# Performance work log

Hardware: AMD Instinct MI355X
Metric: run time of the kernel (lower is better)

## Reference

```python
import jax, jax.numpy as jnp
import numpy as np
import math

B, S, HID, H = 4, 2048, 1024, 16
D = HID // H


def setup_inputs() -> dict:
    key = jax.random.key(0)
    ks = jax.random.split(key, 13)
    xavier = lambda k: jax.random.normal(k, (HID, HID), jnp.float32) * math.sqrt(2.0 / (HID + HID))
    return {
        "q": jax.random.normal(ks[0], (B, S, HID), jnp.float32),
        "k": jax.random.normal(ks[1], (B, S, HID), jnp.float32),
        "v": jax.random.normal(ks[2], (B, S, HID), jnp.float32),
        "padding_mask": jax.random.randint(ks[3], (B, S), 0, 2, jnp.int32),
        "Wq": xavier(ks[4]), "bq": jnp.zeros((HID,), jnp.float32),
        "Wk": xavier(ks[5]), "bk": jnp.zeros((HID,), jnp.float32),
        "Wv": xavier(ks[6]), "bv": jnp.zeros((HID,), jnp.float32),
        "Wo": xavier(ks[7]), "bo": jnp.zeros((HID,), jnp.float32),
        "is_causal": 1,
    }


def reference(q, k, v, padding_mask, Wq, bq, Wk, bk, Wv, bv, Wo, bo, is_causal):
    b, s, _ = q.shape
    # torch Linear: y = x @ W.T + b; reshape to [B, H, S, D]
    proj = lambda x, W, bias: (x @ W.T + bias).reshape(b, s, H, D).transpose(0, 2, 1, 3)
    qh, kh, vh = proj(q, Wq, bq), proj(k, Wk, bk), proj(v, Wv, bv)
    corr = jnp.einsum("bhqd,bhkd->bhqk", qh, kh) / math.sqrt(D)  # [B,H,S,S]
    # padding_mask.view(B,1,S,1): masks QUERY rows where mask == 0 (faithful to source)
    corr = jnp.where(padding_mask[:, None, :, None] == 0, jnp.float32(-1e9), corr)
    if is_causal:
        # triu -inf above diagonal; where(...) equals corr + (-inf) at masked slots
        tri = jnp.triu(jnp.ones((s, s), bool), k=1)
        corr = jnp.where(tri[None, None], -jnp.inf, corr)
    prob = jax.nn.softmax(corr, axis=-1)  # dropout p=0 (eval)
    hidden = jnp.einsum("bhqk,bhkd->bhqd", prob, vh)  # [B,H,S,D]
    hidden = hidden.transpose(0, 2, 1, 3).reshape(b, s, H * D)
    return hidden @ Wo.T + bo
```

## Files before the change

### kernel.cpp

```cpp
#include <hip/hip_runtime.h>
#include <hip/hip_bf16.h>
#include <stdint.h>

typedef __attribute__((ext_vector_type(8))) short bf16x8;
typedef __attribute__((ext_vector_type(4))) float f32x4;
typedef __attribute__((ext_vector_type(16))) float f32x16;
typedef __attribute__((ext_vector_type(8))) unsigned short ushort8;
typedef __attribute__((ext_vector_type(4))) unsigned short ushort4v;
typedef __attribute__((ext_vector_type(4))) unsigned int u32x4;
typedef __attribute__((ext_vector_type(2))) unsigned int u32x2;

#define DEVINL __device__ __forceinline__

static constexpr int BB  = 4;
static constexpr int SS  = 2048;
static constexpr int HID = 1024;
static constexpr int NH  = 16;
static constexpr int DH  = 64;

DEVINL unsigned short f2bf(float f) {
  unsigned u = __builtin_bit_cast(unsigned, f);
  u += 0x7fffu + ((u >> 16) & 1u);
  return (unsigned short)(u >> 16);
}

DEVINL unsigned cvt_pk_bf16(float lo, float hi) {
  unsigned r;
  asm("v_cvt_pk_bf16_f32 %0, %1, %2" : "=v"(r) : "v"(lo), "v"(hi));
  return r;
}

DEVINL void gload_lds16(const void* g, void* lds) {
  __builtin_amdgcn_global_load_lds(
      (__attribute__((address_space(1))) unsigned int*)(g),
      (__attribute__((address_space(3))) unsigned int*)(lds), 16, 0, 0);
}

__global__ void cvt4_weights(const float* __restrict__ a,
                             const float* __restrict__ b,
                             const float* __restrict__ c,
                             const float* __restrict__ d,
                             unsigned short* __restrict__ dst) {
  int which = blockIdx.x >> 10;
  const float* src = which == 0 ? a : which == 1 ? b : which == 2 ? c : d;
  int i = ((blockIdx.x & 1023) * 256 + threadIdx.x) * 4;
  float4 v = *(const float4*)(src + i);
  ushort4v h;
  h.x = f2bf(v.x); h.y = f2bf(v.y); h.z = f2bf(v.z); h.w = f2bf(v.w);
  *(ushort4v*)(dst + which * 1048576 + i) = h;
}

template <int A_F32, int OUT_F32>
__launch_bounds__(256)
__global__ void gemm_bt(const void* __restrict__ Ap,
                        const unsigned short* __restrict__ Bw,
                        const float* __restrict__ bias,
                        void* __restrict__ Cp, int M, int N, int K,
                        float oscale) {
  __shared__ __align__(16) unsigned char As[16384];
  __shared__ __align__(16) unsigned char Bs[16384];
  const int cpx = gridDim.x >> 3;
  const int bid = (blockIdx.x & 7) * cpx + (blockIdx.x >> 3);
  const int nb = N >> 7;
  const int bm = bid / nb, bn = bid % nb;
  const int m0 = bm << 7, n0 = bn << 7;
  const int t = threadIdx.x, lane = t & 63, wv = t >> 6;
  const int wr = wv >> 1, wc = wv & 1;
  const int l15 = lane & 15, l4 = lane >> 4;

  f32x4 acc[4][4] = {};

  for (int k0 = 0; k0 < K; k0 += 64) {
#pragma unroll
    for (int j = 0; j < 4; ++j) {
      int p = (wv * 4 + j) * 1024 + lane * 16;
      int row = p >> 7;
      int cb = (p & 127) ^ ((row & 7) << 4);
      gload_lds16(Bw + (size_t)(n0 + row) * K + k0 + (cb >> 1),
                  Bs + (wv * 4 + j) * 1024);
    }
    if (A_F32) {
      const float* Af = (const float*)Ap;
#pragma unroll
      for (int j = 0; j < 8; ++j) {
        int qid = t + j * 256;
        int row = qid >> 4;
        int q16 = qid & 15;
        float4 v = *(const float4*)(Af + (size_t)(m0 + row) * K + k0 + q16 * 4);
        u32x2 w;
        w.x = cvt_pk_bf16(v.x, v.y);
        w.y = cvt_pk_bf16(v.z, v.w);
        int byte = (row * 128 + q16 * 8) ^ ((row & 7) << 4);
        *(u32x2*)(As + byte) = w;
      }
    } else {
      const unsigned short* Ab = (const unsigned short*)Ap;
#pragma unroll
      for (int j = 0; j < 4; ++j) {
        int p = (wv * 4 + j) * 1024 + lane * 16;
        int row = p >> 7;
        int cb = (p & 127) ^ ((row & 7) << 4);
        gload_lds16(Ab + (size_t)(m0 + row) * K + k0 + (cb >> 1),
                    As + (wv * 4 + j) * 1024);
      }
    }
    asm volatile("s_waitcnt vmcnt(0)" ::: "memory");
    __syncthreads();

    bf16x8 af[2][4], bfr[2][4];
#pragma unroll
    for (int kh = 0; kh < 2; ++kh) {
#pragma unroll
      for (int m = 0; m < 4; ++m) {
        int r = wr * 64 + m * 16 + l15;
        int byte = (r * 128 + kh * 64 + l4 * 16) ^ ((r & 7) << 4);
        af[kh][m] = *(const bf16x8*)(As + byte);
      }
#pragma unroll
      for (int n = 0; n < 4; ++n) {
        int r = wc * 64 + n * 16 + l15;
        int byte = (r * 128 + kh * 64 + l4 * 16) ^ ((r & 7) << 4);
        bfr[kh][n] = *(const bf16x8*)(Bs + byte);
      }
    }
#pragma unroll
    for (int kh = 0; kh < 2; ++kh)
#pragma unroll
      for (int m = 0; m < 4; ++m)
#pragma unroll
        for (int n = 0; n < 4; ++n)
          acc[m][n] = __builtin_amdgcn_mfma_f32_16x16x32_bf16(
              af[kh][m], bfr[kh][n], acc[m][n], 0, 0, 0);
    __syncthreads();
  }

#pragma unroll
  for (int n = 0; n < 4; ++n) {
    int col = n0 + wc * 64 + n * 16 + l15;
    float bc = bias[col];
#pragma unroll
    for (int m = 0; m < 4; ++m) {
      int rowb = m0 + wr * 64 + m * 16 + l4 * 4;
#pragma unroll
      for (int r = 0; r < 4; ++r) {
        float val = (acc[m][n][r] + bc) * oscale;
        if (OUT_F32)
          ((float*)Cp)[(size_t)(rowb + r) * N + col] = val;
        else
          ((unsigned short*)Cp)[(size_t)(rowb + r) * N + col] = f2bf(val);
      }
    }
  }
}

__launch_bounds__(256)
__global__ void transpose_v(const unsigned short* __restrict__ Vh,
                            unsigned short* __restrict__ Vt) {
  __shared__ unsigned short Ts[64][65];
  const int bid = blockIdx.x;
  const int st = bid & 31, h = (bid >> 5) & 15, b = bid >> 9;
  const int s0 = st << 6;
  const int t = threadIdx.x;
  {
    int si = t >> 2, jq = (t & 3) * 16;
    const unsigned short* src =
        Vh + ((size_t)(b * SS + s0 + si)) * HID + h * DH + jq;
    ushort8 v0 = *(const ushort8*)src;
    ushort8 v1 = *(const ushort8*)(src + 8);
#pragma unroll
    for (int e = 0; e < 8; ++e) {
      Ts[si][jq + e] = v0[e];
      Ts[si][jq + 8 + e] = v1[e];
    }
  }
  __syncthreads();
  {
    int d = t >> 2, sq = (t & 3) * 16;
    ushort8 o0, o1;
#pragma unroll
    for (int e = 0; e < 8; ++e) {
      o0[e] = Ts[sq + e][d];
      o1[e] = Ts[sq + 8 + e][d];
    }
    unsigned short* dst =
        Vt + ((size_t)((b * NH + h) * DH + d)) * SS + s0 + sq;
    *(ushort8*)dst = o0;
    *(ushort8*)(dst + 8) = o1;
  }
}

__launch_bounds__(256)
__global__ void attn_kernel(const unsigned short* __restrict__ Qh,
                            const unsigned short* __restrict__ Kh,
                            const unsigned short* __restrict__ Vt,
                            const int* __restrict__ pad,
                            const int* __restrict__ pcausal,
                            unsigned short* __restrict__ Out) {
  __shared__ __align__(16) unsigned char Ks[2][8192];
  __shared__ __align__(16) unsigned char Vs[2][8192];
  const int bid = (blockIdx.x & 7) * 64 + (blockIdx.x >> 3);
  const int pr = bid & 7, h = (bid >> 3) & 15, b = bid >> 7;
  const int t = threadIdx.x, lane = t & 63, wv = t >> 6;
  const int l31 = lane & 31, hi = lane >> 5;
  const int causal = *pcausal;
  const int sw = (l31 & 7) << 4;

  for (int half = 0; half < 2; ++half) {
    const int qt = half ? (15 - pr) : pr;
    const int q0 = qt << 7;
    const int qrow = q0 + wv * 32 + l31;
    const bool padded = (pad[b * SS + qrow] == 0);

    const unsigned short* Qb = Qh + ((size_t)(b * SS) + qrow) * HID + h * DH;
    bf16x8 qf[4];
#pragma unroll
    for (int dd = 0; dd < 4; ++dd) {
      qf[dd] = *(const bf16x8*)(Qb + dd * 16 + hi * 8);
      if (padded) qf[dd] = (bf16x8)0;
    }

    f32x16 oacc[2] = {};
    float m = -__builtin_inff(), l = 0.f;
    const int nkt = causal ? (2 * qt + 2) : (SS >> 6);

    auto STAGE = [&](int kt, int s) {
#pragma unroll
      for (int j = 0; j < 2; ++j) {
        int pb = (wv * 2 + j) * 1024 + lane * 16;
        int r_ = pb >> 7;
        int cb = (pb & 127) ^ ((r_ & 7) << 4);
        gload_lds16(Kh + ((size_t)(b * SS) + (kt << 6) + r_) * HID + h * DH +
                        (cb >> 1),
                    Ks[s] + (wv * 2 + j) * 1024);
        gload_lds16(Vt + ((size_t)((b * NH + h) * DH + r_)) * SS + (kt << 6) +
                        (cb >> 1),
                    Vs[s] + (wv * 2 + j) * 1024);
      }
    };

    if (half) __syncthreads();
    STAGE(0, 0);
    for (int kt = 0; kt < nkt; ++kt) {
      asm volatile("s_waitcnt vmcnt(0)" ::: "memory");
      __syncthreads();
      if (kt + 1 < nkt) STAGE(kt + 1, (kt + 1) & 1);
      const unsigned char* Kb = Ks[kt & 1];
      const unsigned char* Vb = Vs[kt & 1];
      const int k0 = kt << 6;

      const bool active = (!causal) || (k0 <= q0 + wv * 32 + 31);
      if (active) {
        f32x16 sacc[2] = {};
#pragma unroll
        for (int kb = 0; kb < 2; ++kb) {
#pragma unroll
          for (int dd = 0; dd < 4; ++dd) {
            int krow = kb * 32 + l31;
            int byte = (krow * 128 + dd * 32 + hi * 16) ^ sw;
            bf16x8 kf = *(const bf16x8*)(Kb + byte);
            sacc[kb] = __builtin_amdgcn_mfma_f32_32x32x16_bf16(kf, qf[dd],
                                                               sacc[kb], 0, 0, 0);
          }
        }
        if (causal && (k0 + 63 > q0 + wv * 32)) {
#pragma unroll
          for (int kb = 0; kb < 2; ++kb)
#pragma unroll
            for (int r = 0; r < 16; ++r) {
              int kidx = k0 + kb * 32 + (r & 3) + 8 * (r >> 2) + 4 * hi;
              if (kidx > qrow) sacc[kb][r] = -__builtin_inff();
            }
        }
        float ta = fmaxf(sacc[0][0], sacc[0][1]);
        float tb = fmaxf(sacc[0][2], sacc[0][3]);
#pragma unroll
        for (int r = 4; r < 16; r += 4) {
          ta = fmaxf(ta, fmaxf(sacc[0][r], sacc[0][r + 1]));
          tb = fmaxf(tb, fmaxf(sacc[0][r + 2], sacc[0][r + 3]));
        }
#pragma unroll
        for (int r = 0; r < 16; r += 4) {
          ta = fmaxf(ta, fmaxf(sacc[1][r], sacc[1][r + 1]));
          tb = fmaxf(tb, fmaxf(sacc[1][r + 2], sacc[1][r + 3]));
        }
        float tmax = fmaxf(ta, tb);
        tmax = fmaxf(tmax, __shfl_xor(tmax, 32));
        if (__any(tmax > m + 8.0f)) {
          float mnew = fmaxf(m, tmax);
          float corr = __builtin_amdgcn_exp2f(m - mnew);
          m = mnew;
          l *= corr;
#pragma unroll
          for (int db = 0; db < 2; ++db)
#pragma unroll
            for (int r = 0; r < 16; ++r) oacc[db][r] *= corr;
        }
        float ls = 0.f;
#pragma unroll
        for (int kb = 0; kb < 2; ++kb)
#pragma unroll
          for (int r = 0; r < 16; ++r) {
            float p = __builtin_amdgcn_exp2f(sacc[kb][r] - m);
            sacc[kb][r] = p;
            ls += p;
          }
        l += ls;

        bf16x8 pf[4];
#pragma unroll
        for (int kb = 0; kb < 2; ++kb) {
          unsigned w0 = cvt_pk_bf16(sacc[kb][0], sacc[kb][1]);
          unsigned w1 = cvt_pk_bf16(sacc[kb][2], sacc[kb][3]);
          unsigned w2 = cvt_pk_bf16(sacc[kb][4], sacc[kb][5]);
          unsigned w3 = cvt_pk_bf16(sacc[kb][6], sacc[kb][7]);
          unsigned w4 = cvt_pk_bf16(sacc[kb][8], sacc[kb][9]);
          unsigned w5 = cvt_pk_bf16(sacc[kb][10], sacc[kb][11]);
          unsigned w6 = cvt_pk_bf16(sacc[kb][12], sacc[kb][13]);
          unsigned w7 = cvt_pk_bf16(sacc[kb][14], sacc[kb][15]);
          unsigned t0 = __shfl_xor(hi ? w0 : w2, 32);
          unsigned t1 = __shfl_xor(hi ? w1 : w3, 32);
          unsigned t2 = __shfl_xor(hi ? w4 : w6, 32);
          unsigned t3 = __shfl_xor(hi ? w5 : w7, 32);
          u32x4 lo, hf;
          lo[0] = hi ? t0 : w0;
          lo[1] = hi ? t1 : w1;
          lo[2] = hi ? w2 : t0;
          lo[3] = hi ? w3 : t1;
          hf[0] = hi ? t2 : w4;
          hf[1] = hi ? t3 : w5;
          hf[2] = hi ? w6 : t2;
          hf[3] = hi ? w7 : t3;
          pf[2 * kb] = __builtin_bit_cast(bf16x8, lo);
          pf[2 * kb + 1] = __builtin_bit_cast(bf16x8, hf);
        }
#pragma unroll
        for (int db = 0; db < 2; ++db) {
#pragma unroll
          for (int kk = 0; kk < 4; ++kk) {
            int drow = db * 32 + l31;
            int byte = (drow * 128 + kk * 32 + hi * 16) ^ sw;
            bf16x8 vf = *(const bf16x8*)(Vb + byte);
            oacc[db] = __builtin_amdgcn_mfma_f32_32x32x16_bf16(vf, pf[kk],
                                                               oacc[db], 0, 0, 0);
          }
        }
      }
    }

    float ltot = l + __shfl_xor(l, 32);
    float inv = 1.0f / ltot;
    size_t rowoff = ((size_t)(b * SS) + qrow) * HID + h * DH;
#pragma unroll
    for (int db = 0; db < 2; ++db) {
#pragma unroll
      for (int g = 0; g < 4; ++g) {
        ushort4v o;
#pragma unroll
        for (int j = 0; j < 4; ++j) o[j] = f2bf(oacc[db][4 * g + j] * inv);
        *(ushort4v*)(Out + rowoff + db * 32 + 8 * g + 4 * hi) = o;
      }
    }
  }
}

extern "C" void kernel_launch(void* const* d_in, const int* in_sizes, int n_in,
                              void* d_out, int out_size, void* d_ws,
                              size_t ws_size, hipStream_t stream) {
  const float* q = (const float*)d_in[0];
  const float* k = (const float*)d_in[1];
  const float* v = (const float*)d_in[2];
  const int* pad = (const int*)d_in[3];
  const float* Wq = (const float*)d_in[4];
  const float* bq = (const float*)d_in[5];
  const float* Wk = (const float*)d_in[6];
  const float* bk = (const float*)d_in[7];
  const float* Wv = (const float*)d_in[8];
  const float* bv = (const float*)d_in[9];
  const float* Wo = (const float*)d_in[10];
  const float* bo = (const float*)d_in[11];
  const int* iscausal = (const int*)d_in[12];
  float* out = (float*)d_out;

  const float SCL = 0.18033688011112042f;
  const int NQKV = BB * SS * HID;

  unsigned short* Wqb = (unsigned short*)d_ws;
  unsigned short* Wkb = Wqb + 1048576;
  unsigned short* Wvb = Wkb + 1048576;
  unsigned short* Wob = Wvb + 1048576;
  unsigned short* Qh = Wob + 1048576;
  unsigned short* Kh = Qh + (size_t)NQKV;
  unsigned short* Vtp = Kh + (size_t)NQKV;
  unsigned short* Htmp = Vtp + (size_t)NQKV;

  cvt4_weights<<<4096, 256, 0, stream>>>(Wq, Wk, Wv, Wo, Wqb);

  gemm_bt<1, 0><<<512, 256, 0, stream>>>(q, Wqb, bq, Qh, 8192, 1024, 1024, SCL);
  gemm_bt<1, 0><<<512, 256, 0, stream>>>(k, Wkb, bk, Kh, 8192, 1024, 1024, 1.0f);
  gemm_bt<1, 0><<<512, 256, 0, stream>>>(v, Wvb, bv, Htmp, 8192, 1024, 1024, 1.0f);

  transpose_v<<<2048, 256, 0, stream>>>(Htmp, Vtp);

  attn_kernel<<<512, 256, 0, stream>>>(Qh, Kh, Vtp, pad, iscausal, Htmp);

  gemm_bt<0, 1><<<512, 256, 0, stream>>>(Htmp, Wob, bo, out, 8192, 1024, 1024,
                                         1.0f);
}
```

Measured before the change: 200.4 us.

## Merge QKV projections into one launch and use 128-key attention tiles

The three Q/K/V projection GEMMs become a single 1536-block launch that picks input, weight, bias and scale per block, and the templated GEMM is split into dedicated QKV and output kernels. The attention kernel now stages 128 keys per pipeline step (two 64-key sub-blocks) with bigger double-buffered K/V LDS tiles and a 256-byte-row swizzle for V. The aim is to cut launch gaps and tail effects across the projections and to halve the number of barrier/staging rounds in attention. The cost is double the LDS per attention block, which may lower occupancy, and coarser causal work at the diagonal.

```diff
diff --git a/kernel.cpp b/kernel.cpp
--- a/kernel.cpp
+++ b/kernel.cpp
@@ -50,13 +50,108 @@
   *(ushort4v*)(dst + which * 1048576 + i) = h;
 }
 
-template <int A_F32, int OUT_F32>
 __launch_bounds__(256)
-__global__ void gemm_bt(const void* __restrict__ Ap,
-                        const unsigned short* __restrict__ Bw,
-                        const float* __restrict__ bias,
-                        void* __restrict__ Cp, int M, int N, int K,
-                        float oscale) {
+__global__ void gemm_qkv(const float* __restrict__ qp,
+                         const float* __restrict__ kp,
+                         const float* __restrict__ vp,
+                         const unsigned short* __restrict__ W,
+                         const float* __restrict__ bq,
+                         const float* __restrict__ bk,
+                         const float* __restrict__ bv,
+                         unsigned short* __restrict__ dstAll, float sclq) {
+  __shared__ __align__(16) unsigned char As[16384];
+  __shared__ __align__(16) unsigned char Bs[16384];
+  const int cpx = gridDim.x >> 3;
+  const int bid = (blockIdx.x & 7) * cpx + (blockIdx.x >> 3);
+  const int which = bid / 512;
+  const int tile = bid - which * 512;
+  const int bm = tile >> 3, bn = tile & 7;
+  const int m0 = bm << 7, n0 = bn << 7;
+  const int K = 1024, N = 1024;
+  const float* Af = which == 0 ? qp : which == 1 ? kp : vp;
+  const unsigned short* Bw = W + which * 1048576;
+  const float* bias = which == 0 ? bq : which == 1 ? bk : bv;
+  const float osc = which == 0 ? sclq : 1.0f;
+  unsigned short* Cp = dstAll + (size_t)which * 8388608;
+
+  const int t = threadIdx.x, lane = t & 63, wv = t >> 6;
+  const int wr = wv >> 1, wc = wv & 1;
+  const int l15 = lane & 15, l4 = lane >> 4;
+
+  f32x4 acc[4][4] = {};
+
+  for (int k0 = 0; k0 < K; k0 += 64) {
+#pragma unroll
+    for (int j = 0; j < 4; ++j) {
+      int p = (wv * 4 + j) * 1024 + lane * 16;
+      int row = p >> 7;
+      int cb = (p & 127) ^ ((row & 7) << 4);
+      gload_lds16(Bw + (size_t)(n0 + row) * K + k0 + (cb >> 1),
+                  Bs + (wv * 4 + j) * 1024);
+    }
+#pragma unroll
+    for (int j = 0; j < 8; ++j) {
+      int qid = t + j * 256;
+      int row = qid >> 4;
+      int q16 = qid & 15;
+      float4 v = *(const float4*)(Af + (size_t)(m0 + row) * K + k0 + q16 * 4);
+      u32x2 w;
+      w.x = cvt_pk_bf16(v.x, v.y);
+      w.y = cvt_pk_bf16(v.z, v.w);
+      int byte = (row * 128 + q16 * 8) ^ ((row & 7) << 4);
+      *(u32x2*)(As + byte) = w;
+    }
+    asm volatile("s_waitcnt vmcnt(0)" ::: "memory");
+    __syncthreads();
+
+    bf16x8 af[2][4], bfr[2][4];
+#pragma unroll
+    for (int kh = 0; kh < 2; ++kh) {
+#pragma unroll
+      for (int m = 0; m < 4; ++m) {
+        int r = wr * 64 + m * 16 + l15;
+        int byte = (r * 128 + kh * 64 + l4 * 16) ^ ((r & 7) << 4);
+        af[kh][m] = *(const bf16x8*)(As + byte);
+      }
+#pragma unroll
+      for (int n = 0; n < 4; ++n) {
+        int r = wc * 64 + n * 16 + l15;
+        int byte = (r * 128 + kh * 64 + l4 * 16) ^ ((r & 7) << 4);
+        bfr[kh][n] = *(const bf16x8*)(Bs + byte);
+      }
+    }
+#pragma unroll
+    for (int kh = 0; kh < 2; ++kh)
+#pragma unroll
+      for (int m = 0; m < 4; ++m)
+#pragma unroll
+        for (int n = 0; n < 4; ++n)
+          acc[m][n] = __builtin_amdgcn_mfma_f32_16x16x32_bf16(
+              af[kh][m], bfr[kh][n], acc[m][n], 0, 0, 0);
+    __syncthreads();
+  }
+
+#pragma unroll
+  for (int n = 0; n < 4; ++n) {
+    int col = n0 + wc * 64 + n * 16 + l15;
+    float bc = bias[col];
+#pragma unroll
+    for (int m = 0; m < 4; ++m) {
+      int rowb = m0 + wr * 64 + m * 16 + l4 * 4;
+#pragma unroll
+      for (int r = 0; r < 4; ++r) {
+        float val = (acc[m][n][r] + bc) * osc;
+        Cp[(size_t)(rowb + r) * N + col] = f2bf(val);
+      }
+    }
+  }
+}
+
+__launch_bounds__(256)
+__global__ void gemm_out(const unsigned short* __restrict__ Ab,
+                         const unsigned short* __restrict__ Bw,
+                         const float* __restrict__ bias,
+                         float* __restrict__ Cp, int M, int N, int K) {
   __shared__ __align__(16) unsigned char As[16384];
   __shared__ __align__(16) unsigned char Bs[16384];
   const int cpx = gridDim.x >> 3;
@@ -78,31 +173,8 @@
       int cb = (p & 127) ^ ((row & 7) << 4);
       gload_lds16(Bw + (size_t)(n0 + row) * K + k0 + (cb >> 1),
                   Bs + (wv * 4 + j) * 1024);
-    }
-    if (A_F32) {
-      const float* Af = (const float*)Ap;
-#pragma unroll
-      for (int j = 0; j < 8; ++j) {
-        int qid = t + j * 256;
-        int row = qid >> 4;
-        int q16 = qid & 15;
-        float4 v = *(const float4*)(Af + (size_t)(m0 + row) * K + k0 + q16 * 4);
-        u32x2 w;
-        w.x = cvt_pk_bf16(v.x, v.y);
-        w.y = cvt_pk_bf16(v.z, v.w);
-        int byte = (row * 128 + q16 * 8) ^ ((row & 7) << 4);
-        *(u32x2*)(As + byte) = w;
-      }
-    } else {
-      const unsigned short* Ab = (const unsigned short*)Ap;
-#pragma unroll
-      for (int j = 0; j < 4; ++j) {
-        int p = (wv * 4 + j) * 1024 + lane * 16;
-        int row = p >> 7;
-        int cb = (p & 127) ^ ((row & 7) << 4);
-        gload_lds16(Ab + (size_t)(m0 + row) * K + k0 + (cb >> 1),
-                    As + (wv * 4 + j) * 1024);
-      }
+      gload_lds16(Ab + (size_t)(m0 + row) * K + k0 + (cb >> 1),
+                  As + (wv * 4 + j) * 1024);
     }
     asm volatile("s_waitcnt vmcnt(0)" ::: "memory");
     __syncthreads();
@@ -142,13 +214,8 @@
     for (int m = 0; m < 4; ++m) {
       int rowb = m0 + wr * 64 + m * 16 + l4 * 4;
 #pragma unroll
-      for (int r = 0; r < 4; ++r) {
-        float val = (acc[m][n][r] + bc) * oscale;
-        if (OUT_F32)
-          ((float*)Cp)[(size_t)(rowb + r) * N + col] = val;
-        else
-          ((unsigned short*)Cp)[(size_t)(rowb + r) * N + col] = f2bf(val);
-      }
+      for (int r = 0; r < 4; ++r)
+        Cp[(size_t)(rowb + r) * N + col] = acc[m][n][r] + bc;
     }
   }
 }
@@ -196,14 +263,13 @@
                             const int* __restrict__ pad,
                             const int* __restrict__ pcausal,
                             unsigned short* __restrict__ Out) {
-  __shared__ __align__(16) unsigned char Ks[2][8192];
-  __shared__ __align__(16) unsigned char Vs[2][8192];
+  __shared__ __align__(16) unsigned char Ks[2][16384];
+  __shared__ __align__(16) unsigned char Vs[2][16384];
   const int bid = (blockIdx.x & 7) * 64 + (blockIdx.x >> 3);
   const int pr = bid & 7, h = (bid >> 3) & 15, b = bid >> 7;
   const int t = threadIdx.x, lane = t & 63, wv = t >> 6;
   const int l31 = lane & 31, hi = lane >> 5;
   const int causal = *pcausal;
-  const int sw = (l31 & 7) << 4;
 
   for (int half = 0; half < 2; ++half) {
     const int qt = half ? (15 - pr) : pr;
@@ -221,20 +287,22 @@
 
     f32x16 oacc[2] = {};
     float m = -__builtin_inff(), l = 0.f;
-    const int nkt = causal ? (2 * qt + 2) : (SS >> 6);
+    const int nkt = causal ? (qt + 1) : (SS >> 7);
 
     auto STAGE = [&](int kt, int s) {
 #pragma unroll
-      for (int j = 0; j < 2; ++j) {
-        int pb = (wv * 2 + j) * 1024 + lane * 16;
-        int r_ = pb >> 7;
-        int cb = (pb & 127) ^ ((r_ & 7) << 4);
-        gload_lds16(Kh + ((size_t)(b * SS) + (kt << 6) + r_) * HID + h * DH +
-                        (cb >> 1),
-                    Ks[s] + (wv * 2 + j) * 1024);
-        gload_lds16(Vt + ((size_t)((b * NH + h) * DH + r_)) * SS + (kt << 6) +
-                        (cb >> 1),
-                    Vs[s] + (wv * 2 + j) * 1024);
+      for (int j = 0; j < 4; ++j) {
+        int p = (wv * 4 + j) * 1024 + lane * 16;
+        int kr = p >> 7;
+        int kcb = (p & 127) ^ ((kr & 7) << 4);
+        gload_lds16(Kh + ((size_t)(b * SS) + (kt << 7) + kr) * HID + h * DH +
+                        (kcb >> 1),
+                    Ks[s] + (wv * 4 + j) * 1024);
+        int vr = p >> 8;
+        int vcb = (p & 255) ^ ((vr & 15) << 4);
+        gload_lds16(Vt + ((size_t)((b * NH + h) * DH + vr)) * SS + (kt << 7) +
+                        (vcb >> 1),
+                    Vs[s] + (wv * 4 + j) * 1024);
       }
     };
 
@@ -246,17 +314,19 @@
       if (kt + 1 < nkt) STAGE(kt + 1, (kt + 1) & 1);
       const unsigned char* Kb = Ks[kt & 1];
       const unsigned char* Vb = Vs[kt & 1];
-      const int k0 = kt << 6;
-
-      const bool active = (!causal) || (k0 <= q0 + wv * 32 + 31);
-      if (active) {
+
+#pragma unroll
+      for (int sub = 0; sub < 2; ++sub) {
+        const int k0 = (kt << 7) + (sub << 6);
+        const bool active = (!causal) || (k0 <= q0 + wv * 32 + 31);
+        if (!active) continue;
         f32x16 sacc[2] = {};
 #pragma unroll
         for (int kb = 0; kb < 2; ++kb) {
 #pragma unroll
           for (int dd = 0; dd < 4; ++dd) {
-            int krow = kb * 32 + l31;
-            int byte = (krow * 128 + dd * 32 + hi * 16) ^ sw;
+            int krow = sub * 64 + kb * 32 + l31;
+            int byte = (krow * 128 + dd * 32 + hi * 16) ^ ((krow & 7) << 4);
             bf16x8 kf = *(const bf16x8*)(Kb + byte);
             sacc[kb] = __builtin_amdgcn_mfma_f32_32x32x16_bf16(kf, qf[dd],
                                                                sacc[kb], 0, 0, 0);
@@ -338,7 +408,8 @@
 #pragma unroll
           for (int kk = 0; kk < 4; ++kk) {
             int drow = db * 32 + l31;
-            int byte = (drow * 128 + kk * 32 + hi * 16) ^ sw;
+            int byte = (drow * 256 + sub * 128 + kk * 32 + hi * 16) ^
+                       ((drow & 15) << 4);
             bf16x8 vf = *(const bf16x8*)(Vb + byte);
             oacc[db] = __builtin_amdgcn_mfma_f32_32x32x16_bf16(vf, pf[kk],
                                                                oacc[db], 0, 0, 0);
@@ -384,25 +455,22 @@
   const float SCL = 0.18033688011112042f;
   const int NQKV = BB * SS * HID;
 
-  unsigned short* Wqb = (unsigned short*)d_ws;
-  unsigned short* Wkb = Wqb + 1048576;
-  unsigned short* Wvb = Wkb + 1048576;
-  unsigned short* Wob = Wvb + 1048576;
-  unsigned short* Qh = Wob + 1048576;
-  unsigned short* Kh = Qh + (size_t)NQKV;
-  unsigned short* Vtp = Kh + (size_t)NQKV;
-  unsigned short* Htmp = Vtp + (size_t)NQKV;
-
-  cvt4_weights<<<4096, 256, 0, stream>>>(Wq, Wk, Wv, Wo, Wqb);
-
-  gemm_bt<1, 0><<<512, 256, 0, stream>>>(q, Wqb, bq, Qh, 8192, 1024, 1024, SCL);
-  gemm_bt<1, 0><<<512, 256, 0, stream>>>(k, Wkb, bk, Kh, 8192, 1024, 1024, 1.0f);
-  gemm_bt<1, 0><<<512, 256, 0, stream>>>(v, Wvb, bv, Htmp, 8192, 1024, 1024, 1.0f);
-
-  transpose_v<<<2048, 256, 0, stream>>>(Htmp, Vtp);
+  unsigned short* Wcat = (unsigned short*)d_ws;
+  unsigned short* Wob = Wcat + 3145728;
+  unsigned short* QKVh = Wob + 1048576;
+  unsigned short* Qh = QKVh;
+  unsigned short* Kh = QKVh + (size_t)NQKV;
+  unsigned short* Vh = QKVh + 2 * (size_t)NQKV;
+  unsigned short* Vtp = QKVh + 3 * (size_t)NQKV;
+  unsigned short* Htmp = Vh;
+
+  cvt4_weights<<<4096, 256, 0, stream>>>(Wq, Wk, Wv, Wo, Wcat);
+
+  gemm_qkv<<<1536, 256, 0, stream>>>(q, k, v, Wcat, bq, bk, bv, QKVh, SCL);
+
+  transpose_v<<<2048, 256, 0, stream>>>(Vh, Vtp);
 
   attn_kernel<<<512, 256, 0, stream>>>(Qh, Kh, Vtp, pad, iscausal, Htmp);
 
-  gemm_bt<0, 1><<<512, 256, 0, stream>>>(Htmp, Wob, bo, out, 8192, 1024, 1024,
-                                         1.0f);
-}
+  gemm_out<<<512, 256, 0, stream>>>(Htmp, Wob, bo, out, 8192, 1024, 1024);
+}
```

After: 188.8 us. -5.8%, faster.

## Double-buffer GEMM LDS tiles and widen attention KV tiles to 128

Applied to the files above, without the earlier changes.

The projection GEMM now double-buffers its A and B LDS tiles, prefetching the next K-slice (fp32 A goes through registers) while computing the current one, which also drops one barrier per iteration. The attention kernel stages 128-key K/V tiles instead of 64 and processes them as two 64-key sub-steps, halving the number of barrier and stage rounds. V's LDS layout changes to 256-byte rows with a 16-row swizzle. LDS use doubles in both kernels, which may lower occupancy, and the A prefetch adds register pressure. The workspace pointer renaming is cosmetic.

```diff
diff --git a/kernel.cpp b/kernel.cpp
--- a/kernel.cpp
+++ b/kernel.cpp
@@ -57,8 +57,8 @@
                         const float* __restrict__ bias,
                         void* __restrict__ Cp, int M, int N, int K,
                         float oscale) {
-  __shared__ __align__(16) unsigned char As[16384];
-  __shared__ __align__(16) unsigned char Bs[16384];
+  __shared__ __align__(16) unsigned char As[2][16384];
+  __shared__ __align__(16) unsigned char Bs[2][16384];
   const int cpx = gridDim.x >> 3;
   const int bid = (blockIdx.x & 7) * cpx + (blockIdx.x >> 3);
   const int nb = N >> 7;
@@ -67,45 +67,60 @@
   const int t = threadIdx.x, lane = t & 63, wv = t >> 6;
   const int wr = wv >> 1, wc = wv & 1;
   const int l15 = lane & 15, l4 = lane >> 4;
+  const float* Af = (const float*)Ap;
+  const unsigned short* Ab = (const unsigned short*)Ap;
 
   f32x4 acc[4][4] = {};
-
-  for (int k0 = 0; k0 < K; k0 += 64) {
+  float4 ar[8];
+
+  auto LOAD_A = [&](int k0) {
+#pragma unroll
+    for (int j = 0; j < 8; ++j) {
+      int qid = t + j * 256;
+      int row = qid >> 4;
+      int q16 = qid & 15;
+      ar[j] = *(const float4*)(Af + (size_t)(m0 + row) * K + k0 + q16 * 4);
+    }
+  };
+  auto WRITE_A = [&](int s) {
+#pragma unroll
+    for (int j = 0; j < 8; ++j) {
+      int qid = t + j * 256;
+      int row = qid >> 4;
+      int q16 = qid & 15;
+      u32x2 w;
+      w.x = cvt_pk_bf16(ar[j].x, ar[j].y);
+      w.y = cvt_pk_bf16(ar[j].z, ar[j].w);
+      int byte = (row * 128 + q16 * 8) ^ ((row & 7) << 4);
+      *(u32x2*)(As[s] + byte) = w;
+    }
+  };
+  auto STAGE = [&](int k0, int s) {
 #pragma unroll
     for (int j = 0; j < 4; ++j) {
       int p = (wv * 4 + j) * 1024 + lane * 16;
       int row = p >> 7;
       int cb = (p & 127) ^ ((row & 7) << 4);
       gload_lds16(Bw + (size_t)(n0 + row) * K + k0 + (cb >> 1),
-                  Bs + (wv * 4 + j) * 1024);
-    }
-    if (A_F32) {
-      const float* Af = (const float*)Ap;
-#pragma unroll
-      for (int j = 0; j < 8; ++j) {
-        int qid = t + j * 256;
-        int row = qid >> 4;
-        int q16 = qid & 15;
-        float4 v = *(const float4*)(Af + (size_t)(m0 + row) * K + k0 + q16 * 4);
-        u32x2 w;
-        w.x = cvt_pk_bf16(v.x, v.y);
-        w.y = cvt_pk_bf16(v.z, v.w);
-        int byte = (row * 128 + q16 * 8) ^ ((row & 7) << 4);
-        *(u32x2*)(As + byte) = w;
-      }
-    } else {
-      const unsigned short* Ab = (const unsigned short*)Ap;
-#pragma unroll
-      for (int j = 0; j < 4; ++j) {
-        int p = (wv * 4 + j) * 1024 + lane * 16;
-        int row = p >> 7;
-        int cb = (p & 127) ^ ((row & 7) << 4);
+                  Bs[s] + (wv * 4 + j) * 1024);
+      if (!A_F32)
         gload_lds16(Ab + (size_t)(m0 + row) * K + k0 + (cb >> 1),
-                    As + (wv * 4 + j) * 1024);
-      }
-    }
+                    As[s] + (wv * 4 + j) * 1024);
+    }
+  };
+
+  if (A_F32) LOAD_A(0);
+  STAGE(0, 0);
+  const int nk = K >> 6;
+  for (int i = 0; i < nk; ++i) {
+    const int s = i & 1;
+    if (A_F32) WRITE_A(s);
     asm volatile("s_waitcnt vmcnt(0)" ::: "memory");
     __syncthreads();
+    if (i + 1 < nk) {
+      if (A_F32) LOAD_A((i + 1) << 6);
+      STAGE((i + 1) << 6, s ^ 1);
+    }
 
     bf16x8 af[2][4], bfr[2][4];
 #pragma unroll
@@ -114,13 +129,13 @@
       for (int m = 0; m < 4; ++m) {
         int r = wr * 64 + m * 16 + l15;
         int byte = (r * 128 + kh * 64 + l4 * 16) ^ ((r & 7) << 4);
-        af[kh][m] = *(const bf16x8*)(As + byte);
+        af[kh][m] = *(const bf16x8*)(As[s] + byte);
       }
 #pragma unroll
       for (int n = 0; n < 4; ++n) {
         int r = wc * 64 + n * 16 + l15;
         int byte = (r * 128 + kh * 64 + l4 * 16) ^ ((r & 7) << 4);
-        bfr[kh][n] = *(const bf16x8*)(Bs + byte);
+        bfr[kh][n] = *(const bf16x8*)(Bs[s] + byte);
       }
     }
 #pragma unroll
@@ -131,7 +146,6 @@
         for (int n = 0; n < 4; ++n)
           acc[m][n] = __builtin_amdgcn_mfma_f32_16x16x32_bf16(
               af[kh][m], bfr[kh][n], acc[m][n], 0, 0, 0);
-    __syncthreads();
   }
 
 #pragma unroll
@@ -196,14 +210,13 @@
                             const int* __restrict__ pad,
                             const int* __restrict__ pcausal,
                             unsigned short* __restrict__ Out) {
-  __shared__ __align__(16) unsigned char Ks[2][8192];
-  __shared__ __align__(16) unsigned char Vs[2][8192];
+  __shared__ __align__(16) unsigned char Ks[2][16384];
+  __shared__ __align__(16) unsigned char Vs[2][16384];
   const int bid = (blockIdx.x & 7) * 64 + (blockIdx.x >> 3);
   const int pr = bid & 7, h = (bid >> 3) & 15, b = bid >> 7;
   const int t = threadIdx.x, lane = t & 63, wv = t >> 6;
   const int l31 = lane & 31, hi = lane >> 5;
   const int causal = *pcausal;
-  const int sw = (l31 & 7) << 4;
 
   for (int half = 0; half < 2; ++half) {
     const int qt = half ? (15 - pr) : pr;
@@ -221,20 +234,22 @@
 
     f32x16 oacc[2] = {};
     float m = -__builtin_inff(), l = 0.f;
-    const int nkt = causal ? (2 * qt + 2) : (SS >> 6);
+    const int nkt = causal ? (qt + 1) : (SS >> 7);
 
     auto STAGE = [&](int kt, int s) {
 #pragma unroll
-      for (int j = 0; j < 2; ++j) {
-        int pb = (wv * 2 + j) * 1024 + lane * 16;
-        int r_ = pb >> 7;
-        int cb = (pb & 127) ^ ((r_ & 7) << 4);
-        gload_lds16(Kh + ((size_t)(b * SS) + (kt << 6) + r_) * HID + h * DH +
-                        (cb >> 1),
-                    Ks[s] + (wv * 2 + j) * 1024);
-        gload_lds16(Vt + ((size_t)((b * NH + h) * DH + r_)) * SS + (kt << 6) +
-                        (cb >> 1),
-                    Vs[s] + (wv * 2 + j) * 1024);
+      for (int j = 0; j < 4; ++j) {
+        int p = (wv * 4 + j) * 1024 + lane * 16;
+        int kr = p >> 7;
+        int kcb = (p & 127) ^ ((kr & 7) << 4);
+        gload_lds16(Kh + ((size_t)(b * SS) + (kt << 7) + kr) * HID + h * DH +
+                        (kcb >> 1),
+                    Ks[s] + (wv * 4 + j) * 1024);
+        int vr = p >> 8;
+        int vcb = (p & 255) ^ ((vr & 15) << 4);
+        gload_lds16(Vt + ((size_t)((b * NH + h) * DH + vr)) * SS + (kt << 7) +
+                        (vcb >> 1),
+                    Vs[s] + (wv * 4 + j) * 1024);
       }
     };
 
@@ -246,17 +261,19 @@
       if (kt + 1 < nkt) STAGE(kt + 1, (kt + 1) & 1);
       const unsigned char* Kb = Ks[kt & 1];
       const unsigned char* Vb = Vs[kt & 1];
-      const int k0 = kt << 6;
-
-      const bool active = (!causal) || (k0 <= q0 + wv * 32 + 31);
-      if (active) {
+
+#pragma unroll
+      for (int sub = 0; sub < 2; ++sub) {
+        const int k0 = (kt << 7) + (sub << 6);
+        const bool active = (!causal) || (k0 <= q0 + wv * 32 + 31);
+        if (!active) continue;
         f32x16 sacc[2] = {};
 #pragma unroll
         for (int kb = 0; kb < 2; ++kb) {
 #pragma unroll
           for (int dd = 0; dd < 4; ++dd) {
-            int krow = kb * 32 + l31;
-            int byte = (krow * 128 + dd * 32 + hi * 16) ^ sw;
+            int krow = sub * 64 + kb * 32 + l31;
+            int byte = (krow * 128 + dd * 32 + hi * 16) ^ ((krow & 7) << 4);
             bf16x8 kf = *(const bf16x8*)(Kb + byte);
             sacc[kb] = __builtin_amdgcn_mfma_f32_32x32x16_bf16(kf, qf[dd],
                                                                sacc[kb], 0, 0, 0);
@@ -338,7 +355,8 @@
 #pragma unroll
           for (int kk = 0; kk < 4; ++kk) {
             int drow = db * 32 + l31;
-            int byte = (drow * 128 + kk * 32 + hi * 16) ^ sw;
+            int byte = (drow * 256 + sub * 128 + kk * 32 + hi * 16) ^
+                       ((drow & 15) << 4);
             bf16x8 vf = *(const bf16x8*)(Vb + byte);
             oacc[db] = __builtin_amdgcn_mfma_f32_32x32x16_bf16(vf, pf[kk],
                                                                oacc[db], 0, 0, 0);
@@ -384,22 +402,24 @@
   const float SCL = 0.18033688011112042f;
   const int NQKV = BB * SS * HID;
 
-  unsigned short* Wqb = (unsigned short*)d_ws;
-  unsigned short* Wkb = Wqb + 1048576;
-  unsigned short* Wvb = Wkb + 1048576;
-  unsigned short* Wob = Wvb + 1048576;
+  unsigned short* Wcat = (unsigned short*)d_ws;
+  unsigned short* Wob = Wcat + 3145728;
   unsigned short* Qh = Wob + 1048576;
   unsigned short* Kh = Qh + (size_t)NQKV;
-  unsigned short* Vtp = Kh + (size_t)NQKV;
-  unsigned short* Htmp = Vtp + (size_t)NQKV;
-
-  cvt4_weights<<<4096, 256, 0, stream>>>(Wq, Wk, Wv, Wo, Wqb);
-
-  gemm_bt<1, 0><<<512, 256, 0, stream>>>(q, Wqb, bq, Qh, 8192, 1024, 1024, SCL);
-  gemm_bt<1, 0><<<512, 256, 0, stream>>>(k, Wkb, bk, Kh, 8192, 1024, 1024, 1.0f);
-  gemm_bt<1, 0><<<512, 256, 0, stream>>>(v, Wvb, bv, Htmp, 8192, 1024, 1024, 1.0f);
-
-  transpose_v<<<2048, 256, 0, stream>>>(Htmp, Vtp);
+  unsigned short* Vh = Kh + (size_t)NQKV;
+  unsigned short* Vtp = Vh + (size_t)NQKV;
+  unsigned short* Htmp = Vh;
+
+  cvt4_weights<<<4096, 256, 0, stream>>>(Wq, Wk, Wv, Wo, Wcat);
+
+  gemm_bt<1, 0><<<512, 256, 0, stream>>>(q, Wcat, bq, Qh, 8192, 1024, 1024,
+                                         SCL);
+  gemm_bt<1, 0><<<512, 256, 0, stream>>>(k, Wcat + 1048576, bk, Kh, 8192, 1024,
+                                         1024, 1.0f);
+  gemm_bt<1, 0><<<512, 256, 0, stream>>>(v, Wcat + 2097152, bv, Vh, 8192, 1024,
+                                         1024, 1.0f);
+
+  transpose_v<<<2048, 256, 0, stream>>>(Vh, Vtp);
 
   attn_kernel<<<512, 256, 0, stream>>>(Qh, Kh, Vtp, pad, iscausal, Htmp);
 
```

Result: no change. 200.3 us (-0.1%).
